# Kernel optimization log

Measured on AMD Instinct MI355X. Metric: run time of the kernel, lower is better.

## Reference

```python
import jax, jax.numpy as jnp
import numpy as np

N, E, DIN, DH, DOUT, NB = 50000, 400000, 32, 128, 16, 2

def setup_inputs() -> dict:
    key = jax.random.key(0)
    ks = jax.random.split(key, 16)
    s = 0.05
    inp = {
        "inputs": jax.random.normal(ks[0], (N, DIN), jnp.float32),
        "frames": jax.random.normal(ks[1], (N, 3, 3), jnp.float32),
        "edge_index": jax.random.randint(ks[2], (2, E), 0, N, jnp.int32),
        # GraphNet in/out projections
        "win": jax.random.normal(ks[3], (DIN, DH), jnp.float32) * s,
        "bin_": jnp.zeros((DH,), jnp.float32),
        "wout": jax.random.normal(ks[4], (DH, DOUT), jnp.float32) * s,
        "bout": jnp.zeros((DOUT,), jnp.float32),
        # per-block EdgeConv params, stacked over NB blocks
        # mlp1: Linear(2*DH, DH) -> ReLU -> Linear(DH, DH) -> ReLU -> Linear(DH, DH)
        "w1a": jax.random.normal(ks[5], (NB, 2 * DH, DH), jnp.float32) * s,
        "b1a": jnp.zeros((NB, DH), jnp.float32),
        "w1b": jax.random.normal(ks[6], (NB, DH, DH), jnp.float32) * s,
        "b1b": jnp.zeros((NB, DH), jnp.float32),
        "w1c": jax.random.normal(ks[7], (NB, DH, DH), jnp.float32) * s,
        "b1c": jnp.zeros((NB, DH), jnp.float32),
        # mlp2: Linear(DH, DH) -> ReLU -> Linear(DH, DH)
        "w2a": jax.random.normal(ks[8], (NB, DH, DH), jnp.float32) * s,
        "b2a": jnp.zeros((NB, DH), jnp.float32),
        "w2b": jax.random.normal(ks[9], (NB, DH, DH), jnp.float32) * s,
        "b2b": jnp.zeros((NB, DH), jnp.float32),
    }
    return inp


def reference(inputs, frames, edge_index, win, bin_, wout, bout,
              w1a, b1a, w1b, b1b, w1c, b1c, w2a, b2a, w2b, b2b):
    src = edge_index[0]  # j: message source
    dst = edge_index[1]  # i: aggregation target (PyG convention)
    x = inputs @ win + bin_  # [N, DH]
    for b in range(NB):
        x_j = x[src]  # [E, DH] gather
        x_i = x[dst]  # [E, DH] gather
        m = jnp.concatenate([x_j, x_i], axis=-1)  # [E, 2*DH]
        m = jax.nn.relu(m @ w1a[b] + b1a[b])
        m = jax.nn.relu(m @ w1b[b] + b1b[b])
        m = m @ w1c[b] + b1c[b]  # [E, DH]
        agg = jax.ops.segment_sum(m, dst, num_segments=N)  # aggr='add'
        h = jax.nn.relu(agg @ w2a[b] + b2a[b])
        x = h @ w2b[b] + b2b[b]
    return x @ wout + bout  # [N, DOUT]
```

## Files before the change

kernel.cpp:

```cpp
#include <hip/hip_runtime.h>

#define NN 50000
#define NE 400000
#define DIN 32
#define DH  128
#define DOUT 16
#define NB  2
#define NBLK 49
#define NTILE (NE / 64)

typedef _Float16 half8 __attribute__((ext_vector_type(8)));
typedef _Float16 half4 __attribute__((ext_vector_type(4)));
typedef float    f32x4 __attribute__((ext_vector_type(4)));

#define FENCE() asm volatile("s_waitcnt lgkmcnt(0)" ::: "memory")
#define MFMA16(a, b, c) __builtin_amdgcn_mfma_f32_16x16x32_f16((a), (b), (c), 0, 0, 0)

__global__ void k_prep(const float* __restrict__ w1a, const float* __restrict__ w1b,
                       const float* __restrict__ w1c, const float* __restrict__ w2a,
                       const float* __restrict__ w2b, const float* __restrict__ wout,
                       const float* __restrict__ win, const int* __restrict__ dstI,
                       _Float16* __restrict__ wf, int* __restrict__ deg) {
    const int b = blockIdx.x, tid = threadIdx.x;
    if (b < (NB * 12288) / 256) {
        int c = b * 256 + tid;
        int bb = c / 12288, r = c % 12288;
        int tt = r >> 9, rem = r & 511;
        const float* W; int t;
        if (tt < 8)       { W = w1a + (size_t)bb * 2 * DH * DH; t = tt; }
        else if (tt < 12) { W = w1b + (size_t)bb * DH * DH; t = tt - 8; }
        else if (tt < 16) { W = w1c + (size_t)bb * DH * DH; t = tt - 12; }
        else if (tt < 20) { W = w2a + (size_t)bb * DH * DH; t = tt - 16; }
        else              { W = w2b + (size_t)bb * DH * DH; t = tt - 20; }
        bool perm = (tt >= 12 && tt < 16);
        int n = rem >> 6, l = rem & 63;
        int col = n * 16 + (l & 15);
        half8 v;
#pragma unroll
        for (int j = 0; j < 8; ++j) {
            int row = perm ? ((2 * t + (j >> 2)) * 16 + (l >> 4) * 4 + (j & 3))
                           : (t * 32 + (l >> 4) * 8 + j);
            v[j] = (_Float16)W[(size_t)row * DH + col];
        }
        *(half8*)(wf + (size_t)c * 8) = v;
    } else if (b == 96) {
        int c = tid;
        int t = c >> 6, l = c & 63;
        half8 v;
#pragma unroll
        for (int j = 0; j < 8; ++j)
            v[j] = (_Float16)wout[(size_t)(t * 32 + (l >> 4) * 8 + j) * DOUT + (l & 15)];
        *(half8*)(wf + (size_t)(NB * 12288 + c) * 8) = v;
    } else if (b < 99) {
        int c = (b - 97) * 256 + tid;
        int n = c >> 6, l = c & 63;
        half8 v;
#pragma unroll
        for (int j = 0; j < 8; ++j)
            v[j] = (_Float16)win[(size_t)((l >> 4) * 8 + j) * DH + n * 16 + (l & 15)];
        *(half8*)(wf + (size_t)(NB * 12288 + 256 + c) * 8) = v;
    } else {
        int e = (b - 99) * 256 + tid;
        if (e < NE) atomicAdd(&deg[dstI[e]], 1);
    }
}

__global__ void __launch_bounds__(1024) k_scanA(const int* __restrict__ deg,
                                                int* __restrict__ bsum) {
    __shared__ int ws[16];
    int tid = threadIdx.x, wv = tid >> 6, l = tid & 63;
    int i = blockIdx.x * 1024 + tid;
    int v = (i < NN) ? deg[i] : 0;
#pragma unroll
    for (int off = 32; off; off >>= 1) v += __shfl_down(v, off);
    if (l == 0) ws[wv] = v;
    __syncthreads();
    if (tid == 0) {
        int s = 0;
#pragma unroll
        for (int k = 0; k < 16; ++k) s += ws[k];
        bsum[blockIdx.x] = s;
    }
}

__global__ void k_scanB(const int* __restrict__ bsum, int* __restrict__ boff) {
    int l = threadIdx.x;
    int v = (l < NBLK) ? bsum[l] : 0;
    int s = v;
#pragma unroll
    for (int off = 1; off < 64; off <<= 1) {
        int t = __shfl_up(s, off);
        if (l >= off) s += t;
    }
    if (l < NBLK) boff[l] = s - v;
}

__global__ void __launch_bounds__(1024) k_scanC(const int* __restrict__ deg,
                                                const int* __restrict__ boff,
                                                int* __restrict__ cur) {
    __shared__ int ws[16];
    int tid = threadIdx.x, wv = tid >> 6, l = tid & 63;
    int i = blockIdx.x * 1024 + tid;
    int v = (i < NN) ? deg[i] : 0;
    int s = v;
#pragma unroll
    for (int off = 1; off < 64; off <<= 1) {
        int t = __shfl_up(s, off);
        if (l >= off) s += t;
    }
    if (l == 63) ws[wv] = s;
    __syncthreads();
    if (wv == 0) {
        int t = (l < 16) ? ws[l] : 0;
#pragma unroll
        for (int off = 1; off < 16; off <<= 1) {
            int u = __shfl_up(t, off);
            if (l >= off) t += u;
        }
        if (l < 16) ws[l] = t;
    }
    __syncthreads();
    int base = boff[blockIdx.x] + (wv ? ws[wv - 1] : 0);
    if (i < NN) cur[i] = base + s - v;
}

__global__ void k_scatter(const int* __restrict__ srcI, const int* __restrict__ dstI,
                          int* __restrict__ cur, int* __restrict__ eS,
                          int* __restrict__ eD) {
    int e = blockIdx.x * blockDim.x + threadIdx.x;
    if (e >= NE) return;
    int d = dstI[e];
    int p = atomicAdd(&cur[d], 1);
    eS[p] = srcI[e];
    eD[p] = d;
}

__global__ void __launch_bounds__(256, 4) k_y0(
    const float* __restrict__ inp,
    const half8* __restrict__ winf, const float* __restrict__ bin,
    const half8* __restrict__ wfa, const float* __restrict__ b1a,
    _Float16* __restrict__ yj, _Float16* __restrict__ yi,
    float* __restrict__ agg) {
    __shared__ _Float16 sM[4][2048];
    const int tid = threadIdx.x, wv = tid >> 6, l = tid & 63;
    const int lm = l & 15, lk = l >> 4;
    const int n0 = (blockIdx.x * 4 + wv) * 16;
    if (n0 >= NN) return;
    int node = n0 + lm;
    if (node >= NN) node = NN - 1;

    {
        float4 z4 = make_float4(0.f, 0.f, 0.f, 0.f);
#pragma unroll
        for (int r = 0; r < 4; ++r) {
            int nd = n0 + lk * 4 + r;
            if (nd < NN) {
                float4* q = (float4*)(agg + (size_t)nd * DH + lm * 8);
                q[0] = z4; q[1] = z4;
            }
        }
    }

    const f32x4 z = {0.f, 0.f, 0.f, 0.f};
    half8 a0;
    {
        const float* ip = inp + (size_t)node * DIN + lk * 8;
        float4 v0 = *(const float4*)ip;
        float4 v1 = *(const float4*)(ip + 4);
#pragma unroll
        for (int j = 0; j < 4; ++j) {
            a0[j]     = (_Float16)(&v0.x)[j];
            a0[4 + j] = (_Float16)(&v1.x)[j];
        }
    }
    f32x4 xacc[8];
#pragma unroll
    for (int n = 0; n < 8; ++n) xacc[n] = z;
#pragma unroll
    for (int n = 0; n < 8; ++n) xacc[n] = MFMA16(a0, winf[n * 64 + l], xacc[n]);

    _Float16* sm = sM[wv];
#pragma unroll
    for (int n = 0; n < 8; ++n) {
        float bi = bin[n * 16 + lm];
        int base = ((n >> 1) * 64 + ((n & 1) * 2 + (lm >> 3)) * 16 + lk * 4) * 8 +
                   (lm & 7);
#pragma unroll
        for (int j = 0; j < 4; ++j)
            sm[base + j * 8] = (_Float16)(xacc[n][j] + bi);
    }
    FENCE();

    f32x4 aj[8], ai[8];
#pragma unroll
    for (int n = 0; n < 8; ++n) { aj[n] = z; ai[n] = z; }
#pragma unroll
    for (int t = 0; t < 4; ++t) {
        half8 a = *(const half8*)&sm[(t * 64 + l) * 8];
#pragma unroll
        for (int n = 0; n < 8; ++n) {
            aj[n] = MFMA16(a, wfa[(size_t)(t * 8 + n) * 64 + l], aj[n]);
            ai[n] = MFMA16(a, wfa[(size_t)((t + 4) * 8 + n) * 64 + l], ai[n]);
        }
    }
#pragma unroll
    for (int n = 0; n < 8; ++n) {
        float bi = b1a[n * 16 + lm];
#pragma unroll
        for (int r = 0; r < 4; ++r) {
            int nd = n0 + lk * 4 + r;
            if (nd < NN) {
                yj[(size_t)nd * DH + n * 16 + lm] = (_Float16)aj[n][r];
                yi[(size_t)nd * DH + n * 16 + lm] = (_Float16)(ai[n][r] + bi);
            }
        }
    }
}

__global__ void __launch_bounds__(256, 3) k_edge10(
    const _Float16* __restrict__ yj, const _Float16* __restrict__ yi,
    const int* __restrict__ eS, const int* __restrict__ eD,
    const half8* __restrict__ wfb, const half8* __restrict__ wfc,
    const float* __restrict__ b1b,
    float* __restrict__ agg) {
    __shared__ _Float16 smAll[4][4096];
    __shared__ int slotT[4][16];

    const int tid = threadIdx.x, wv = tid >> 6, l = tid & 63;
    const int lm = l & 15, lk = l >> 4;

    int bid = blockIdx.x;
    int xcd = bid & 7, idx = bid >> 3;
    int tile = (xcd < 2 ? xcd * 782 : 2 * 782 + (xcd - 2) * 781) + idx;
    const int ebase = tile * 64 + wv * 16;

    const int src = eS[ebase + lm];
    const int dst = eD[ebase + lm];

    _Float16* sm = smAll[wv];
    if (lk >= 2) {
        half8 zz;
#pragma unroll
        for (int j = 0; j < 8; ++j) zz[j] = (_Float16)0.f;
#pragma unroll
        for (int g = 0; g < 8; ++g) *(half8*)&sm[(g * 64 + l) * 8] = zz;
    }

    int dprev = __shfl(dst, (l & 48) | ((lm - 1) & 15));
    bool bit = (lm == 0) || (dst != dprev);
    unsigned mask16 = (unsigned)__ballot(bit) & 0xFFFFu;
    int slot_l = __popc(mask16 & ((2u << lm) - 1)) - 1;
    int nsl = __popc(mask16);
    if (l < 16 && bit) slotT[wv][slot_l] = dst;

    half4 bb[8];
#pragma unroll
    for (int n = 0; n < 8; ++n) {
        float4 bf = *(const float4*)(b1b + n * 16 + lk * 4);
#pragma unroll
        for (int r = 0; r < 4; ++r) bb[n][r] = (_Float16)(&bf.x)[r];
    }

    const f32x4 z = {0.f, 0.f, 0.f, 0.f};
    f32x4 acc[8];
#pragma unroll
    for (int n = 0; n < 8; ++n) acc[n] = z;

#pragma unroll
    for (int t = 0; t < 4; ++t) {
        half8 ya = *(const half8*)(yj + (size_t)src * DH + t * 32 + lk * 8);
        half8 yb = *(const half8*)(yi + (size_t)dst * DH + t * 32 + lk * 8);
        half8 m1;
#pragma unroll
        for (int j = 0; j < 8; ++j) {
            _Float16 v = ya[j] + yb[j];
            m1[j] = v > (_Float16)0.f ? v : (_Float16)0.f;
        }
#pragma unroll
        for (int n = 0; n < 8; ++n)
            acc[n] = MFMA16(wfb[(size_t)(t * 8 + n) * 64 + l], m1, acc[n]);
    }

    f32x4 ac3[8];
#pragma unroll
    for (int n = 0; n < 8; ++n) ac3[n] = z;
#pragma unroll
    for (int t = 0; t < 4; ++t) {
        half8 b3;
#pragma unroll
        for (int j = 0; j < 8; ++j) {
            int n2 = 2 * t + (j >> 2), r = j & 3;
            float v = acc[n2][r] + (float)bb[n2][r];
            b3[j] = (_Float16)fmaxf(v, 0.f);
        }
#pragma unroll
        for (int n = 0; n < 8; ++n)
            ac3[n] = MFMA16(wfc[(size_t)(t * 8 + n) * 64 + l], b3, ac3[n]);
    }

#pragma unroll
    for (int n = 0; n < 8; ++n)
#pragma unroll
        for (int r = 0; r < 4; ++r)
            sm[(n * 64 + (lm >> 3) * 16 + lk * 4 + r) * 8 + (lm & 7)] =
                (_Float16)ac3[n][r];
    FENCE();

    half8 ind;
#pragma unroll
    for (int e8 = 0; e8 < 8; ++e8) {
        int ks = lk * 8 + e8;
        int se = __shfl(slot_l, ks & 15);
        ind[e8] = (ks < 16 && se == lm) ? (_Float16)1.f : (_Float16)0.f;
    }
    int4 dv = *(const int4*)&slotT[wv][lk * 4];
#pragma unroll
    for (int g = 0; g < 8; ++g) {
        half8 bf = *(const half8*)&sm[(g * 64 + l) * 8];
        f32x4 p = MFMA16(ind, bf, z);
#pragma unroll
        for (int r = 0; r < 4; ++r) {
            int s0 = lk * 4 + r;
            if (s0 < nsl)
                unsafeAtomicAdd(agg + (size_t)(&dv.x)[r] * DH + g * 16 + lm, p[r]);
        }
    }
}

template <int MODE>
__global__ void __launch_bounds__(256, 3) k_node10(
    float* __restrict__ agg, const int* __restrict__ deg,
    const float* __restrict__ b1c,
    const half8* __restrict__ w2af, const half8* __restrict__ w2bf,
    const float* __restrict__ b2a, const float* __restrict__ b2b,
    const half8* __restrict__ wfaN, const float* __restrict__ b1aN,
    _Float16* __restrict__ yj, _Float16* __restrict__ yi,
    const half8* __restrict__ woutf, const float* __restrict__ bout,
    float* __restrict__ out) {
    __shared__ _Float16 sM[4][2048];
    const int tid = threadIdx.x, wv = tid >> 6, l = tid & 63;
    const int lm = l & 15, lk = l >> 4;
    const int n0 = (blockIdx.x * 4 + wv) * 16;
    if (n0 >= NN) return;
    int nodeA = n0 + lm;
    if (nodeA >= NN) nodeA = NN - 1;
    const float degf = (float)deg[nodeA];

    float b2ar[8], b2br[8];
#pragma unroll
    for (int n = 0; n < 8; ++n) {
        b2ar[n] = b2a[n * 16 + lm];
        b2br[n] = b2b[n * 16 + lm];
    }

    const f32x4 z = {0.f, 0.f, 0.f, 0.f};
    f32x4 acc[8];
#pragma unroll
    for (int n = 0; n < 8; ++n) acc[n] = z;

    for (int t = 0; t < 4; ++t) {
        float* ap = agg + (size_t)nodeA * DH + t * 32 + lk * 8;
        float4 v0 = *(const float4*)ap;
        float4 v1 = *(const float4*)(ap + 4);
        if (MODE == 0) {
            float4 z4 = make_float4(0.f, 0.f, 0.f, 0.f);
            *(float4*)ap = z4;
            *(float4*)(ap + 4) = z4;
        }
        float4 c0 = *(const float4*)(b1c + t * 32 + lk * 8);
        float4 c1 = *(const float4*)(b1c + t * 32 + lk * 8 + 4);
        half8 a;
#pragma unroll
        for (int j = 0; j < 4; ++j) {
            a[j]     = (_Float16)((&v0.x)[j] + degf * (&c0.x)[j]);
            a[4 + j] = (_Float16)((&v1.x)[j] + degf * (&c1.x)[j]);
        }
        const half8* wp = w2af + (size_t)t * 512 + l;
#pragma unroll
        for (int n = 0; n < 8; ++n) acc[n] = MFMA16(a, wp[n * 64], acc[n]);
    }
    _Float16* sm = sM[wv];
#pragma unroll
    for (int n = 0; n < 8; ++n) {
        int base = ((n >> 1) * 64 + ((n & 1) * 2 + (lm >> 3)) * 16 + lk * 4) * 8 +
                   (lm & 7);
#pragma unroll
        for (int j = 0; j < 4; ++j)
            sm[base + j * 8] = (_Float16)fmaxf(acc[n][j] + b2ar[n], 0.f);
    }
    FENCE();
#pragma unroll
    for (int n = 0; n < 8; ++n) acc[n] = z;
    for (int t = 0; t < 4; ++t) {
        half8 a = *(const half8*)&sm[(t * 64 + l) * 8];
        const half8* wp = w2bf + (size_t)t * 512 + l;
#pragma unroll
        for (int n = 0; n < 8; ++n) acc[n] = MFMA16(a, wp[n * 64], acc[n]);
    }
    FENCE();
#pragma unroll
    for (int n = 0; n < 8; ++n) {
        int base = ((n >> 1) * 64 + ((n & 1) * 2 + (lm >> 3)) * 16 + lk * 4) * 8 +
                   (lm & 7);
#pragma unroll
        for (int j = 0; j < 4; ++j)
            sm[base + j * 8] = (_Float16)(acc[n][j] + b2br[n]);
    }
    FENCE();

    if (MODE == 0) {
        f32x4 aj[8], ai[8];
#pragma unroll
        for (int n = 0; n < 8; ++n) { aj[n] = z; ai[n] = z; }
#pragma unroll
        for (int t = 0; t < 4; ++t) {
            half8 a = *(const half8*)&sm[(t * 64 + l) * 8];
#pragma unroll
            for (int n = 0; n < 8; ++n) {
                aj[n] = MFMA16(a, wfaN[(size_t)(t * 8 + n) * 64 + l], aj[n]);
                ai[n] = MFMA16(a, wfaN[(size_t)((t + 4) * 8 + n) * 64 + l], ai[n]);
            }
        }
#pragma unroll
        for (int n = 0; n < 8; ++n) {
            float bi = b1aN[n * 16 + lm];
#pragma unroll
            for (int r = 0; r < 4; ++r) {
                int nd = n0 + lk * 4 + r;
                if (nd < NN) {
                    yj[(size_t)nd * DH + n * 16 + lm] = (_Float16)aj[n][r];
                    yi[(size_t)nd * DH + n * 16 + lm] = (_Float16)(ai[n][r] + bi);
                }
            }
        }
    } else {
        f32x4 ao = z;
        for (int t = 0; t < 4; ++t) {
            half8 a = *(const half8*)&sm[(t * 64 + l) * 8];
            ao = MFMA16(a, woutf[t * 64 + l], ao);
        }
        float bo = bout[lm];
#pragma unroll
        for (int j = 0; j < 4; ++j) {
            int nd = n0 + lk * 4 + j;
            if (nd < NN) out[(size_t)nd * DOUT + lm] = ao[j] + bo;
        }
    }
}

extern "C" void kernel_launch(void* const* d_in, const int* in_sizes, int n_in,
                              void* d_out, int out_size, void* d_ws, size_t ws_size,
                              hipStream_t stream) {
    const float* inputs = (const float*)d_in[0];
    const int* eidx = (const int*)d_in[2];
    const int* srcI = eidx;
    const int* dstI = eidx + NE;
    const float* win  = (const float*)d_in[3];
    const float* bin_ = (const float*)d_in[4];
    const float* wout = (const float*)d_in[5];
    const float* bout = (const float*)d_in[6];
    const float* w1a = (const float*)d_in[7];
    const float* b1a = (const float*)d_in[8];
    const float* w1b = (const float*)d_in[9];
    const float* b1b = (const float*)d_in[10];
    const float* w1c = (const float*)d_in[11];
    const float* b1c = (const float*)d_in[12];
    const float* w2a = (const float*)d_in[13];
    const float* b2a = (const float*)d_in[14];
    const float* w2b = (const float*)d_in[15];
    const float* b2b = (const float*)d_in[16];

    char* p = (char*)d_ws;
    _Float16* yj = (_Float16*)p;    p += (size_t)NN * DH * 2;
    _Float16* yi = (_Float16*)p;    p += (size_t)NN * DH * 2;
    _Float16* wfAll = (_Float16*)p; p += ((size_t)NB * 12288 + 768) * 16;
    float* agg   = (float*)p;       p += (size_t)NN * DH * 4;
    int* deg     = (int*)p;         p += (size_t)NN * 4;
    int* cur     = (int*)p;         p += (size_t)NN * 4;
    int* bsum    = (int*)p;         p += 256;
    int* boff    = (int*)p;         p += 256;
    int* eSrt    = (int*)p;         p += (size_t)NE * 4;
    int* eDrt    = (int*)p;         p += (size_t)NE * 4;
    float* out   = (float*)d_out;

    const half8* wb0 = (const half8*)wfAll;
    const half8* wb1 = (const half8*)(wfAll + (size_t)12288 * 8);
    const half8* wfW = (const half8*)(wfAll + (size_t)NB * 12288 * 8);
    const half8* wfI = (const half8*)(wfAll + (size_t)(NB * 12288 + 256) * 8);

    hipMemsetAsync(deg, 0, (size_t)NN * 4, stream);
    k_prep<<<99 + (NE + 255) / 256, 256, 0, stream>>>(
        w1a, w1b, w1c, w2a, w2b, wout, win, dstI, wfAll, deg);
    k_scanA<<<NBLK, 1024, 0, stream>>>(deg, bsum);
    k_scanB<<<1, 64, 0, stream>>>(bsum, boff);
    k_scanC<<<NBLK, 1024, 0, stream>>>(deg, boff, cur);
    k_scatter<<<(NE + 255) / 256, 256, 0, stream>>>(srcI, dstI, cur, eSrt, eDrt);

    const int NWGN = (NN + 63) / 64;
    k_y0<<<NWGN, 256, 0, stream>>>(inputs, wfI, bin_, wb0, b1a, yj, yi, agg);
    k_edge10<<<NTILE, 256, 0, stream>>>(yj, yi, eSrt, eDrt,
                                        wb0 + 4096, wb0 + 6144, b1b, agg);
    k_node10<0><<<NWGN, 256, 0, stream>>>(
        agg, deg, b1c, wb0 + 8192, wb0 + 10240, b2a, b2b,
        wb1, b1a + DH, yj, yi, nullptr, nullptr, nullptr);
    k_edge10<<<NTILE, 256, 0, stream>>>(yj, yi, eSrt, eDrt,
                                        wb1 + 4096, wb1 + 6144, b1b + DH, agg);
    k_node10<1><<<NWGN, 256, 0, stream>>>(
        agg, deg, b1c + DH, wb1 + 8192, wb1 + 10240, b2a + DH, b2b + DH,
        nullptr, nullptr, nullptr, nullptr, wfW, bout, out);
}
```

Measured before the change: 298.6 us.

## Process multiple edge tiles per workgroup with software-prefetched gathers

The edge kernel now has each workgroup loop over five consecutive 64-edge tiles instead of one, so it launches a fifth as many workgroups. While the current tile's MFMA layers run, each wave issues the next tile's index loads and its yj/yi row gathers. This hides gather latency behind compute and spreads launch and setup costs such as the bias loads. In exchange it holds more live registers under the same launch bounds, and it has coarser load balance across workgroups.

```diff
diff --git a/kernel.cpp b/kernel.cpp
--- a/kernel.cpp
+++ b/kernel.cpp
@@ -8,6 +8,8 @@
 #define NB  2
 #define NBLK 49
 #define NTILE (NE / 64)
+#define TPW   5
+#define NWG_E (NTILE / TPW)
 
 typedef _Float16 half8 __attribute__((ext_vector_type(8)));
 typedef _Float16 half4 __attribute__((ext_vector_type(4)));
@@ -217,7 +219,7 @@
     }
 }
 
-__global__ void __launch_bounds__(256, 3) k_edge10(
+__global__ void __launch_bounds__(256, 3) k_edge12(
     const _Float16* __restrict__ yj, const _Float16* __restrict__ yi,
     const int* __restrict__ eS, const int* __restrict__ eD,
     const half8* __restrict__ wfb, const half8* __restrict__ wfc,
@@ -231,11 +233,8 @@
 
     int bid = blockIdx.x;
     int xcd = bid & 7, idx = bid >> 3;
-    int tile = (xcd < 2 ? xcd * 782 : 2 * 782 + (xcd - 2) * 781) + idx;
-    const int ebase = tile * 64 + wv * 16;
-
-    const int src = eS[ebase + lm];
-    const int dst = eD[ebase + lm];
+    int wg = (xcd < 2 ? xcd * 157 : 2 * 157 + (xcd - 2) * 156) + idx;
+    int ebase = (wg * TPW) * 64 + wv * 16;
 
     _Float16* sm = smAll[wv];
     if (lk >= 2) {
@@ -246,13 +245,6 @@
         for (int g = 0; g < 8; ++g) *(half8*)&sm[(g * 64 + l) * 8] = zz;
     }
 
-    int dprev = __shfl(dst, (l & 48) | ((lm - 1) & 15));
-    bool bit = (lm == 0) || (dst != dprev);
-    unsigned mask16 = (unsigned)__ballot(bit) & 0xFFFFu;
-    int slot_l = __popc(mask16 & ((2u << lm) - 1)) - 1;
-    int nsl = __popc(mask16);
-    if (l < 16 && bit) slotT[wv][slot_l] = dst;
-
     half4 bb[8];
 #pragma unroll
     for (int n = 0; n < 8; ++n) {
@@ -262,68 +254,100 @@
     }
 
     const f32x4 z = {0.f, 0.f, 0.f, 0.f};
-    f32x4 acc[8];
-#pragma unroll
-    for (int n = 0; n < 8; ++n) acc[n] = z;
-
+
+    int src = eS[ebase + lm];
+    int dst = eD[ebase + lm];
+    half8 ya[4], yb[4];
 #pragma unroll
     for (int t = 0; t < 4; ++t) {
-        half8 ya = *(const half8*)(yj + (size_t)src * DH + t * 32 + lk * 8);
-        half8 yb = *(const half8*)(yi + (size_t)dst * DH + t * 32 + lk * 8);
-        half8 m1;
-#pragma unroll
-        for (int j = 0; j < 8; ++j) {
-            _Float16 v = ya[j] + yb[j];
-            m1[j] = v > (_Float16)0.f ? v : (_Float16)0.f;
-        }
+        ya[t] = *(const half8*)(yj + (size_t)src * DH + t * 32 + lk * 8);
+        yb[t] = *(const half8*)(yi + (size_t)dst * DH + t * 32 + lk * 8);
+    }
+
+    for (int i = 0; i < TPW; ++i) {
+        int srcN = 0, dstN = 0;
+        if (i + 1 < TPW) {
+            srcN = eS[ebase + 64 + lm];
+            dstN = eD[ebase + 64 + lm];
+        }
+
+        int dprev = __shfl(dst, (l & 48) | ((lm - 1) & 15));
+        bool bit = (lm == 0) || (dst != dprev);
+        unsigned mask16 = (unsigned)__ballot(bit) & 0xFFFFu;
+        int slot_l = __popc(mask16 & ((2u << lm) - 1)) - 1;
+        int nsl = __popc(mask16);
+        if (l < 16 && bit) slotT[wv][slot_l] = dst;
+
+        f32x4 acc[8];
+#pragma unroll
+        for (int n = 0; n < 8; ++n) acc[n] = z;
+#pragma unroll
+        for (int t = 0; t < 4; ++t) {
+            half8 m1;
+#pragma unroll
+            for (int j = 0; j < 8; ++j) {
+                _Float16 v = ya[t][j] + yb[t][j];
+                m1[j] = v > (_Float16)0.f ? v : (_Float16)0.f;
+            }
+#pragma unroll
+            for (int n = 0; n < 8; ++n)
+                acc[n] = MFMA16(wfb[(size_t)(t * 8 + n) * 64 + l], m1, acc[n]);
+        }
+
+        if (i + 1 < TPW) {
+#pragma unroll
+            for (int t = 0; t < 4; ++t) {
+                ya[t] = *(const half8*)(yj + (size_t)srcN * DH + t * 32 + lk * 8);
+                yb[t] = *(const half8*)(yi + (size_t)dstN * DH + t * 32 + lk * 8);
+            }
+        }
+
+        f32x4 ac3[8];
+#pragma unroll
+        for (int n = 0; n < 8; ++n) ac3[n] = z;
+#pragma unroll
+        for (int t = 0; t < 4; ++t) {
+            half8 b3;
+#pragma unroll
+            for (int j = 0; j < 8; ++j) {
+                int n2 = 2 * t + (j >> 2), r = j & 3;
+                float v = acc[n2][r] + (float)bb[n2][r];
+                b3[j] = (_Float16)fmaxf(v, 0.f);
+            }
+#pragma unroll
+            for (int n = 0; n < 8; ++n)
+                ac3[n] = MFMA16(wfc[(size_t)(t * 8 + n) * 64 + l], b3, ac3[n]);
+        }
+
 #pragma unroll
         for (int n = 0; n < 8; ++n)
-            acc[n] = MFMA16(wfb[(size_t)(t * 8 + n) * 64 + l], m1, acc[n]);
-    }
-
-    f32x4 ac3[8];
-#pragma unroll
-    for (int n = 0; n < 8; ++n) ac3[n] = z;
-#pragma unroll
-    for (int t = 0; t < 4; ++t) {
-        half8 b3;
-#pragma unroll
-        for (int j = 0; j < 8; ++j) {
-            int n2 = 2 * t + (j >> 2), r = j & 3;
-            float v = acc[n2][r] + (float)bb[n2][r];
-            b3[j] = (_Float16)fmaxf(v, 0.f);
-        }
-#pragma unroll
-        for (int n = 0; n < 8; ++n)
-            ac3[n] = MFMA16(wfc[(size_t)(t * 8 + n) * 64 + l], b3, ac3[n]);
-    }
-
-#pragma unroll
-    for (int n = 0; n < 8; ++n)
-#pragma unroll
-        for (int r = 0; r < 4; ++r)
-            sm[(n * 64 + (lm >> 3) * 16 + lk * 4 + r) * 8 + (lm & 7)] =
-                (_Float16)ac3[n][r];
-    FENCE();
-
-    half8 ind;
-#pragma unroll
-    for (int e8 = 0; e8 < 8; ++e8) {
-        int ks = lk * 8 + e8;
-        int se = __shfl(slot_l, ks & 15);
-        ind[e8] = (ks < 16 && se == lm) ? (_Float16)1.f : (_Float16)0.f;
-    }
-    int4 dv = *(const int4*)&slotT[wv][lk * 4];
-#pragma unroll
-    for (int g = 0; g < 8; ++g) {
-        half8 bf = *(const half8*)&sm[(g * 64 + l) * 8];
-        f32x4 p = MFMA16(ind, bf, z);
-#pragma unroll
-        for (int r = 0; r < 4; ++r) {
-            int s0 = lk * 4 + r;
-            if (s0 < nsl)
-                unsafeAtomicAdd(agg + (size_t)(&dv.x)[r] * DH + g * 16 + lm, p[r]);
-        }
+#pragma unroll
+            for (int r = 0; r < 4; ++r)
+                sm[(n * 64 + (lm >> 3) * 16 + lk * 4 + r) * 8 + (lm & 7)] =
+                    (_Float16)ac3[n][r];
+        FENCE();
+
+        half8 ind;
+#pragma unroll
+        for (int e8 = 0; e8 < 8; ++e8) {
+            int ks = lk * 8 + e8;
+            int se = __shfl(slot_l, ks & 15);
+            ind[e8] = (ks < 16 && se == lm) ? (_Float16)1.f : (_Float16)0.f;
+        }
+        int4 dv = *(const int4*)&slotT[wv][lk * 4];
+#pragma unroll
+        for (int g = 0; g < 8; ++g) {
+            half8 bf = *(const half8*)&sm[(g * 64 + l) * 8];
+            f32x4 p = MFMA16(ind, bf, z);
+#pragma unroll
+            for (int r = 0; r < 4; ++r) {
+                int s0 = lk * 4 + r;
+                if (s0 < nsl)
+                    unsafeAtomicAdd(agg + (size_t)(&dv.x)[r] * DH + g * 16 + lm, p[r]);
+            }
+        }
+
+        src = srcN; dst = dstN; ebase += 64;
     }
 }
 
@@ -498,12 +522,12 @@
 
     const int NWGN = (NN + 63) / 64;
     k_y0<<<NWGN, 256, 0, stream>>>(inputs, wfI, bin_, wb0, b1a, yj, yi, agg);
-    k_edge10<<<NTILE, 256, 0, stream>>>(yj, yi, eSrt, eDrt,
+    k_edge12<<<NWG_E, 256, 0, stream>>>(yj, yi, eSrt, eDrt,
                                         wb0 + 4096, wb0 + 6144, b1b, agg);
     k_node10<0><<<NWGN, 256, 0, stream>>>(
         agg, deg, b1c, wb0 + 8192, wb0 + 10240, b2a, b2b,
         wb1, b1a + DH, yj, yi, nullptr, nullptr, nullptr);
-    k_edge10<<<NTILE, 256, 0, stream>>>(yj, yi, eSrt, eDrt,
+    k_edge12<<<NWG_E, 256, 0, stream>>>(yj, yi, eSrt, eDrt,
                                         wb1 + 4096, wb1 + 6144, b1b + DH, agg);
     k_node10<1><<<NWGN, 256, 0, stream>>>(
         agg, deg, b1c + DH, wb1 + 8192, wb1 + 10240, b2a + DH, b2b + DH,
```

Result: slower. 769.6 us (+157.7%).
